# Kernel optimization log

Hardware: AMD Instinct MI355X
Metric: run time of the kernel (lower is better)

The kernel has to match this reference:

```python
import jax, jax.numpy as jnp
import numpy as np
from math import factorial, sqrt

# ---- static configuration (mirrors init_kwargs) ----
IRREPS = [(32, 0), (32, 1), (16, 2)]  # (mul, l); parity of each irrep is (-1)**l (0e,1o,2e)
N_NODES = 200000
DIMS = [m * (2 * l + 1) for m, l in IRREPS]
TOTAL_DIM = sum(DIMS)
OFFS = [0]
for d in DIMS:
    OFFS.append(OFFS[-1] + d)

# ---- real-basis Wigner 3j (same construction as e3nn.o3.wigner_3j) ----
def _cg(j1, m1, j2, m2, j3, m3):
    # su(2) Clebsch-Gordan coefficient <j1 m1 j2 m2 | j3 m3> (Racah formula)
    if m3 != m1 + m2:
        return 0.0
    f = factorial
    pref = sqrt((2 * j3 + 1) * f(j3 + j1 - j2) * f(j3 - j1 + j2) * f(j1 + j2 - j3) / f(j1 + j2 + j3 + 1))
    pref *= sqrt(f(j3 + m3) * f(j3 - m3) * f(j1 - m1) * f(j1 + m1) * f(j2 - m2) * f(j2 + m2))
    s = 0.0
    for k in range(max(0, j2 - j3 - m1, j1 - j3 + m2), min(j1 + j2 - j3, j1 - m1, j2 + m2) + 1):
        s += (-1) ** k / (f(k) * f(j1 + j2 - j3 - k) * f(j1 - m1 - k) * f(j2 + m2 - k) * f(j3 - j2 + m1 + k) * f(j3 - j1 - m2 + k))
    return pref * s

def _q(l):
    # change of basis real <-> complex spherical harmonics, with (-i)**l phase (e3nn convention)
    q = np.zeros((2 * l + 1, 2 * l + 1), dtype=complex)
    for m in range(-l, 0):
        q[l + m, l + abs(m)] = 1 / np.sqrt(2)
        q[l + m, l - abs(m)] = -1j / np.sqrt(2)
    q[l, l] = 1.0
    for m in range(1, l + 1):
        q[l + m, l + abs(m)] = (-1) ** m / np.sqrt(2)
        q[l + m, l - abs(m)] = 1j * (-1) ** m / np.sqrt(2)
    return (-1j) ** l * q

def _w3j(l1, l2, l3):
    C = np.zeros((2 * l1 + 1, 2 * l2 + 1, 2 * l3 + 1))
    for m1 in range(-l1, l1 + 1):
        for m2 in range(-l2, l2 + 1):
            m3 = m1 + m2
            if abs(m3) <= l3:
                C[l1 + m1, l2 + m2, l3 + m3] = _cg(l1, m1, l2, m2, l3, m3)
    W = np.einsum('ai,bj,ck,abc->ijk', _q(l1), _q(l2), np.conj(_q(l3)), C.astype(complex))
    W = np.real(W)
    return (W / np.linalg.norm(W)).astype(np.float32)  # unit Frobenius norm, like e3nn

# ---- enumerate fully-connected TP paths: |l1-l2|<=l3<=l1+l2 and parity match ((-1)**l irreps => l1+l2+l3 even) ----
PATHS = []
for i, (m1, l1) in enumerate(IRREPS):
    for j, (m2, l2) in enumerate(IRREPS):
        for k, (m3, l3) in enumerate(IRREPS):
            if abs(l1 - l2) <= l3 <= l1 + l2 and (l1 + l2 + l3) % 2 == 0:
                PATHS.append((i, j, k))

W3J = {}
for (i, j, k) in PATHS:
    key = (IRREPS[i][1], IRREPS[j][1], IRREPS[k][1])
    if key not in W3J:
        W3J[key] = jnp.asarray(_w3j(*key))

# e3nn normalization: irrep_normalization='component', path_normalization='element', 'uvw' connectivity
FAN = [0] * len(IRREPS)
for (i, j, k) in PATHS:
    FAN[k] += IRREPS[i][0] * IRREPS[j][0]
PATH_COEFF = [sqrt((2 * IRREPS[k][1] + 1) / FAN[k]) for (i, j, k) in PATHS]

TP_WSIZE = sum(IRREPS[i][0] * IRREPS[j][0] * IRREPS[k][0] for (i, j, k) in PATHS)
LIN_WSIZE = sum(m * m for m, l in IRREPS)


def _forward(x, tp_w, lin_w):
    # split x into per-irrep segments [n, mul, 2l+1]
    segs = [x[:, OFFS[i]:OFFS[i + 1]].reshape(-1, IRREPS[i][0], 2 * IRREPS[i][1] + 1)
            for i in range(len(IRREPS))]
    out = [jnp.zeros((x.shape[0], m, 2 * l + 1), x.dtype) for m, l in IRREPS]
    # FullyConnectedTensorProduct(x, x): one CG contraction per path
    off = 0
    for (i, j, k), coeff in zip(PATHS, PATH_COEFF):
        m1, l1 = IRREPS[i]; m2, l2 = IRREPS[j]; m3, l3 = IRREPS[k]
        n = m1 * m2 * m3
        w = tp_w[off:off + n].reshape(m1, m2, m3); off += n
        C = W3J[(l1, l2, l3)]
        out[k] = out[k] + coeff * jnp.einsum('uvw,ijk,zui,zvj->zwk', w, C, segs[i], segs[j])
    # o3.Linear skip: per-irrep channel mixing, 1/sqrt(fan_in) normalization
    loff = 0
    for idx, (m, l) in enumerate(IRREPS):
        w = lin_w[loff:loff + m * m].reshape(m, m); loff += m * m
        out[idx] = out[idx] + jnp.einsum('uw,zui->zwi', w, segs[idx]) / sqrt(m)
    return jnp.concatenate([o.reshape(o.shape[0], -1) for o in out], axis=1)


def setup_inputs() -> dict:
    key = jax.random.key(0)
    k1, k2, k3 = jax.random.split(key, 3)
    return {
        "x": jax.random.normal(k1, (N_NODES, TOTAL_DIM), dtype=jnp.float32),
        "tp_w": jax.random.normal(k2, (TP_WSIZE,), dtype=jnp.float32),
        "lin_w": jax.random.normal(k3, (LIN_WSIZE,), dtype=jnp.float32),
    }


def reference(x, tp_w, lin_w):
    return _forward(x, tp_w, lin_w)
```

## Files before the change

### kernel.cpp

```cpp
#include <hip/hip_runtime.h>

#define T000 0
#define T011 1
#define T101 10
#define T110 19
#define T022 28
#define T202 53
#define T220 78
#define T121 103
#define T211 148
#define T112 193
#define T222 238
#define NTAB 363

#define TP000 0
#define TP011 32768
#define TP022 65536
#define TP101 73728
#define TP110 106496
#define TP112 139264
#define TP121 155648
#define TP202 172032
#define TP211 180224
#define TP220 196608
#define TP222 204800
#define TPEND 208896

#define OFF_CW000 512
#define OFF_CW110 17408
#define OFF_CW220 34304
#define OFF_CW011 38656
#define OFF_CW121 71424
#define OFF_CW022 87808
#define OFF_CW112 96000
#define OFF_CW222 104448
#define OFF_LIN0  106624
#define OFF_LIN1  107648
#define OFF_LIN2  108672
#define PREP_THREADS 108416
#define XT_BYTE_OFF ((size_t)1 << 20)

struct cplx { double re, im; };
__device__ inline cplx cmul(cplx a, cplx b){ return {a.re*b.re - a.im*b.im, a.re*b.im + a.im*b.re}; }

__device__ double dfact(int n){ double r=1; for(int i=2;i<=n;i++) r*=i; return r; }

__device__ double dcgc(int j1,int m1,int j2,int m2,int j3,int m3){
  if (m3 != m1+m2) return 0.0;
  double pref = sqrt((2.0*j3+1)*dfact(j3+j1-j2)*dfact(j3-j1+j2)*dfact(j1+j2-j3)/dfact(j1+j2+j3+1));
  pref *= sqrt(dfact(j3+m3)*dfact(j3-m3)*dfact(j1-m1)*dfact(j1+m1)*dfact(j2-m2)*dfact(j2+m2));
  int k0 = max(0, max(j2-j3-m1, j1-j3+m2));
  int k1 = min(j1+j2-j3, min(j1-m1, j2+m2));
  double s = 0.0;
  for(int k=k0;k<=k1;k++){
    double d = dfact(k)*dfact(j1+j2-j3-k)*dfact(j1-m1-k)*dfact(j2+m2-k)*dfact(j3-j2+m1+k)*dfact(j3-j1-m2+k);
    s += ((k&1)?-1.0:1.0)/d;
  }
  return pref*s;
}

__device__ cplx qel(int l, int a, int c){
  const double s2 = 0.7071067811865475244;
  cplx base = {0.0, 0.0};
  if (a < l){
    if (c == 2*l-a) base = {s2, 0.0};
    else if (c == a) base = {0.0, -s2};
  } else if (a == l){
    if (c == l) base = {1.0, 0.0};
  } else {
    double sgn = ((a-l)&1)? -1.0 : 1.0;
    if (c == a) base = {sgn*s2, 0.0};
    else if (c == 2*l-a) base = {0.0, sgn*s2};
  }
  cplx ph = {1.0,0.0}, mi = {0.0,-1.0};
  for(int t=0;t<l;t++) ph = cmul(ph, mi);
  return cmul(base, ph);
}

__global__ void w3j_init(float* __restrict__ ws){
  __shared__ double red[128];
  __shared__ double snorm;
  const int spec[11][4] = {
    {0,0,0,T000},{0,1,1,T011},{1,0,1,T101},{1,1,0,T110},
    {0,2,2,T022},{2,0,2,T202},{2,2,0,T220},{1,2,1,T121},
    {2,1,1,T211},{1,1,2,T112},{2,2,2,T222}};
  int tbl = blockIdx.x;
  int l1 = spec[tbl][0], l2 = spec[tbl][1], l3 = spec[tbl][2], off = spec[tbl][3];
  int n1 = 2*l1+1, n2 = 2*l2+1, n3 = 2*l3+1, nel = n1*n2*n3;
  int t = threadIdx.x;
  double val = 0.0;
  if (t < nel){
    int k = t % n3, j = (t/n3) % n2, i = t/(n3*n2);
    for(int a=0;a<n1;a++){ int m1 = a-l1;
      for(int b=0;b<n2;b++){ int m2 = b-l2, m3 = m1+m2;
        if (m3 < -l3 || m3 > l3) continue;
        double C = dcgc(l1,m1,l2,m2,l3,m3);
        if (C == 0.0) continue;
        cplx q1 = qel(l1,a,i), q2 = qel(l2,b,j), q3 = qel(l3,l3+m3,k);
        q3.im = -q3.im;
        cplx p = cmul(cmul(q1,q2), q3);
        val += p.re * C;
      }
    }
  }
  red[t] = val*val;
  __syncthreads();
  for(int s=64; s>0; s>>=1){
    if (t < s) red[t] += red[t+s];
    __syncthreads();
  }
  if (t == 0) snorm = sqrt(red[0]);
  __syncthreads();
  if (t < nel) ws[off + t] = (float)(val / snorm);
}

__device__ inline void pdec(int pid, int m, int& u, int& v){
  int uu = 0;
  while (pid >= m-uu){ pid -= (m-uu); uu++; }
  u = uu; v = uu + pid;
}

__global__ void prep3(const float* __restrict__ tp, const float* __restrict__ lin,
                      float* __restrict__ ws){
  const float PK0 = 1.0f/48.0f;
  const float PK1 = 1.0f/32.0f;
  const float PK2 = sqrtf(5.0f)/48.0f;
  int t = blockIdx.x*256 + threadIdx.x;
  if (t >= PREP_THREADS) return;
  if (t < 16896){
    int w = t & 31, pid = t >> 5; int u,v; pdec(pid,32,u,v);
    float s = tp[TP000+(u*32+v)*32+w];
    if (u < v) s += tp[TP000+(v*32+u)*32+w];
    ws[OFF_CW000 + t] = PK0 * ws[T000] * s; return;
  }
  t -= 16896;
  if (t < 16896){
    int w = t & 31, pid = t >> 5; int u,v; pdec(pid,32,u,v);
    float s = tp[TP110+(u*32+v)*32+w];
    if (u < v) s += tp[TP110+(v*32+u)*32+w];
    ws[OFF_CW110 + 16896 + t - 16896] = PK0 * ws[T110] * s;
    return;
  }
  t -= 16896;
  if (t < 4352){
    int w = t & 31, pid = t >> 5; int u,v; pdec(pid,16,u,v);
    float s = tp[TP220+(u*16+v)*32+w];
    if (u < v) s += tp[TP220+(v*16+u)*32+w];
    ws[OFF_CW220 + t] = PK0 * ws[T220] * s; return;
  }
  t -= 4352;
  if (t < 32768){
    int w = t & 31, r = t >> 5; int p = r & 31, q = r >> 5;
    float d011 = ws[T011], d101 = ws[T101];
    float s = d011 * tp[TP011+(p*32+q)*32+w] + d101 * tp[TP101+(q*32+p)*32+w];
    ws[OFF_CW011 + t] = PK1 * s; return;
  }
  t -= 32768;
  if (t < 16384){
    int w = t & 31, r = t >> 5; int q = r & 31, b = r >> 5;
    float s = tp[TP121+(q*16+b)*32+w] + tp[TP211+(b*32+q)*32+w];
    ws[OFF_CW121 + t] = PK1 * s; return;
  }
  t -= 16384;
  if (t < 8192){
    int w = t & 15, r = t >> 4; int p = r & 31, b = r >> 5;
    float d022 = ws[T022], d202 = ws[T202];
    float s = d022 * tp[TP022+(p*16+b)*16+w] + d202 * tp[TP202+(b*32+p)*16+w];
    ws[OFF_CW022 + t] = PK2 * s; return;
  }
  t -= 8192;
  if (t < 8448){
    int w = t & 15, pid = t >> 4; int u,v; pdec(pid,32,u,v);
    float s = tp[TP112+(u*32+v)*16+w];
    if (u < v) s += tp[TP112+(v*32+u)*16+w];
    ws[OFF_CW112 + t] = PK2 * s; return;
  }
  t -= 8448;
  if (t < 2176){
    int w = t & 15, pid = t >> 4; int u,v; pdec(pid,16,u,v);
    float s = tp[TP222+(u*16+v)*16+w];
    if (u < v) s += tp[TP222+(v*16+u)*16+w];
    ws[OFF_CW222 + t] = PK2 * s; return;
  }
  t -= 2176;
  if (t < 1024){ ws[OFF_LIN0 + t] = 0.17677669529663687f * lin[t]; return; }
  t -= 1024;
  if (t < 1024){ ws[OFF_LIN1 + t] = 0.17677669529663687f * lin[1024+t]; return; }
  t -= 1024;
  ws[OFF_LIN2 + t] = 0.25f * lin[2048+t];
}

__global__ void transpose_kernel(const float* __restrict__ x, float* __restrict__ xt, int N){
  __shared__ float tile[64*209];
  int z0 = blockIdx.x*64;
  int nz = N - z0; if (nz > 64) nz = 64;
  for(int idx=threadIdx.x; idx<64*208; idx+=256){
    int zl = idx/208, d = idx - zl*208;
    float v = (zl < nz) ? x[(size_t)z0*208 + idx] : 0.f;
    tile[zl*209 + d] = v;
  }
  __syncthreads();
  for(int idx=threadIdx.x; idx<64*208; idx+=256){
    int d = idx>>6, zl = idx & 63;
    if (zl < nz) xt[(size_t)d*N + z0 + zl] = tile[zl*209 + d];
  }
}

__global__ __launch_bounds__(256, 4)
void tp_fused(const float* __restrict__ xt, const float* __restrict__ ws,
              float* __restrict__ out, int N, int NB){
  __shared__ float sT[NTAB];
  for(int i=threadIdx.x; i<NTAB; i+=256) sT[i] = ws[i];
  __syncthreads();
  int phase = blockIdx.x / NB;
  int z = (blockIdx.x % NB)*256 + threadIdx.x;
  if (z >= N) return;
  const size_t Ns = (size_t)N;
#define XT(d) xt[(size_t)(d)*Ns + z]
  float* __restrict__ oz = out + (size_t)z*208;

  if (phase == 0){
    float acc[32];
#pragma unroll
    for(int w=0;w<32;w++) acc[w]=0.f;
    const float* wp = ws + OFF_CW000;
#pragma unroll 1
    for(int u=0;u<32;u++){
      float su = XT(u);
#pragma unroll 1
      for(int v=u;v<32;v++){
        float p = su * XT(v);
#pragma unroll
        for(int w=0;w<32;w++) acc[w] = fmaf(p, wp[w], acc[w]);
        wp += 32;
      }
    }
    const float* lw = ws + OFF_LIN0;
#pragma unroll 1
    for(int u=0;u<32;u++){
      float su = XT(u);
#pragma unroll
      for(int w=0;w<32;w++) acc[w] = fmaf(su, lw[w], acc[w]);
      lw += 32;
    }
    wp = ws + OFF_CW110;
#pragma unroll 1
    for(int u=0;u<32;u++){
      float a0=XT(32+3*u), a1=XT(33+3*u), a2=XT(34+3*u);
#pragma unroll 1
      for(int v=u;v<32;v++){
        float p = a0*XT(32+3*v) + a1*XT(33+3*v) + a2*XT(34+3*v);
#pragma unroll
        for(int w=0;w<32;w++) acc[w] = fmaf(p, wp[w], acc[w]);
        wp += 32;
      }
    }
    wp = ws + OFF_CW220;
#pragma unroll 1
    for(int u=0;u<16;u++){
      float b0=XT(128+5*u),b1=XT(129+5*u),b2=XT(130+5*u),b3=XT(131+5*u),b4=XT(132+5*u);
#pragma unroll 1
      for(int v=u;v<16;v++){
        float p = b0*XT(128+5*v)+b1*XT(129+5*v)+b2*XT(130+5*v)+b3*XT(131+5*v)+b4*XT(132+5*v);
#pragma unroll
        for(int w=0;w<32;w++) acc[w] = fmaf(p, wp[w], acc[w]);
        wp += 32;
      }
    }
#pragma unroll
    for(int w=0;w<32;w++) oz[w] = acc[w];

  } else if (phase == 1){
    float acc[96];
#pragma unroll
    for(int i=0;i<96;i++) acc[i]=0.f;
    const float* wp = ws + OFF_CW011;
#pragma unroll 1
    for(int q=0;q<32;q++){
      float vq0=XT(32+3*q), vq1=XT(33+3*q), vq2=XT(34+3*q);
#pragma unroll 1
      for(int p=0;p<32;p++){
        float sp = XT(p);
        float p0=sp*vq0, p1=sp*vq1, p2=sp*vq2;
#pragma unroll
        for(int w=0;w<32;w++){
          float wt = wp[w];
          acc[3*w  ] = fmaf(p0, wt, acc[3*w  ]);
          acc[3*w+1] = fmaf(p1, wt, acc[3*w+1]);
          acc[3*w+2] = fmaf(p2, wt, acc[3*w+2]);
        }
        wp += 32;
      }
    }
    wp = ws + OFF_CW121;
#pragma unroll 1
    for(int b=0;b<16;b++){
      float t0=XT(128+5*b),t1=XT(129+5*b),t2=XT(130+5*b),t3=XT(131+5*b),t4=XT(132+5*b);
      float q9[9];
#pragma unroll
      for(int a=0;a<3;a++)
#pragma unroll
        for(int c=0;c<3;c++){
          float s = sT[T121+(a*5+0)*3+c]*t0 + sT[T121+(a*5+1)*3+c]*t1
                  + sT[T121+(a*5+2)*3+c]*t2 + sT[T121+(a*5+3)*3+c]*t3
                  + sT[T121+(a*5+4)*3+c]*t4;
          q9[a*3+c] = s;
        }
#pragma unroll 1
      for(int q=0;q<32;q++){
        float v0=XT(32+3*q), v1=XT(33+3*q), v2=XT(34+3*q);
        float p0 = v0*q9[0] + v1*q9[3] + v2*q9[6];
        float p1 = v0*q9[1] + v1*q9[4] + v2*q9[7];
        float p2 = v0*q9[2] + v1*q9[5] + v2*q9[8];
#pragma unroll
        for(int w=0;w<32;w++){
          float wt = wp[w];
          acc[3*w  ] = fmaf(p0, wt, acc[3*w  ]);
          acc[3*w+1] = fmaf(p1, wt, acc[3*w+1]);
          acc[3*w+2] = fmaf(p2, wt, acc[3*w+2]);
        }
        wp += 32;
      }
    }
    const float* lw = ws + OFF_LIN1;
#pragma unroll 1
    for(int u=0;u<32;u++){
      float v0=XT(32+3*u), v1=XT(33+3*u), v2=XT(34+3*u);
#pragma unroll
      for(int w=0;w<32;w++){
        float wt = lw[w];
        acc[3*w  ] = fmaf(v0, wt, acc[3*w  ]);
        acc[3*w+1] = fmaf(v1, wt, acc[3*w+1]);
        acc[3*w+2] = fmaf(v2, wt, acc[3*w+2]);
      }
      lw += 32;
    }
#pragma unroll
    for(int i=0;i<96;i++) oz[32+i] = acc[i];

  } else {
    float acc[80];
#pragma unroll
    for(int i=0;i<80;i++) acc[i]=0.f;
    const float* wp = ws + OFF_CW022;
#pragma unroll 1
    for(int b=0;b<16;b++){
      float t0=XT(128+5*b),t1=XT(129+5*b),t2=XT(130+5*b),t3=XT(131+5*b),t4=XT(132+5*b);
#pragma unroll 1
      for(int p=0;p<32;p++){
        float sp = XT(p);
        float p0=sp*t0,p1=sp*t1,p2=sp*t2,p3=sp*t3,p4=sp*t4;
#pragma unroll
        for(int w=0;w<16;w++){
          float wt = wp[w];
          acc[5*w  ] = fmaf(p0, wt, acc[5*w  ]);
          acc[5*w+1] = fmaf(p1, wt, acc[5*w+1]);
          acc[5*w+2] = fmaf(p2, wt, acc[5*w+2]);
          acc[5*w+3] = fmaf(p3, wt, acc[5*w+3]);
          acc[5*w+4] = fmaf(p4, wt, acc[5*w+4]);
        }
        wp += 16;
      }
    }
    wp = ws + OFF_CW222;
#pragma unroll 1
    for(int u=0;u<16;u++){
      float tu[5];
#pragma unroll
      for(int j=0;j<5;j++) tu[j]=XT(128+5*u+j);
      float r[25];
#pragma unroll
      for(int b=0;b<5;b++)
#pragma unroll
        for(int c=0;c<5;c++){
          float s=0.f;
#pragma unroll
          for(int a=0;a<5;a++) s = fmaf(sT[T222+(a*5+b)*5+c], tu[a], s);
          r[b*5+c]=s;
        }
#pragma unroll 1
      for(int v=u;v<16;v++){
        float s0=XT(128+5*v),s1=XT(129+5*v),s2=XT(130+5*v),s3=XT(131+5*v),s4=XT(132+5*v);
        float p[5];
#pragma unroll
        for(int c=0;c<5;c++) p[c] = s0*r[c]+s1*r[5+c]+s2*r[10+c]+s3*r[15+c]+s4*r[20+c];
#pragma unroll
        for(int w=0;w<16;w++){
          float wt = wp[w];
#pragma unroll
          for(int c=0;c<5;c++) acc[5*w+c] = fmaf(p[c], wt, acc[5*w+c]);
        }
        wp += 16;
      }
    }
    const float* lw = ws + OFF_LIN2;
#pragma unroll 1
    for(int u=0;u<16;u++){
      float t0=XT(128+5*u),t1=XT(129+5*u),t2=XT(130+5*u),t3=XT(131+5*u),t4=XT(132+5*u);
#pragma unroll
      for(int w=0;w<16;w++){
        float wt = lw[w];
        acc[5*w  ] = fmaf(t0, wt, acc[5*w  ]);
        acc[5*w+1] = fmaf(t1, wt, acc[5*w+1]);
        acc[5*w+2] = fmaf(t2, wt, acc[5*w+2]);
        acc[5*w+3] = fmaf(t3, wt, acc[5*w+3]);
        acc[5*w+4] = fmaf(t4, wt, acc[5*w+4]);
      }
      lw += 16;
    }
    wp = ws + OFF_CW112;
#pragma unroll 1
    for(int u=0;u<32;u++){
      float u0=XT(32+3*u), u1=XT(33+3*u), u2=XT(34+3*u);
      float r[15];
#pragma unroll
      for(int b=0;b<3;b++)
#pragma unroll
        for(int c=0;c<5;c++)
          r[b*5+c] = sT[T112+(0*3+b)*5+c]*u0 + sT[T112+(1*3+b)*5+c]*u1
                   + sT[T112+(2*3+b)*5+c]*u2;
#pragma unroll 1
      for(int v=u;v<32;v++){
        float v0=XT(32+3*v), v1=XT(33+3*v), v2=XT(34+3*v);
        float p[5];
#pragma unroll
        for(int c=0;c<5;c++) p[c] = v0*r[c] + v1*r[5+c] + v2*r[10+c];
#pragma unroll
        for(int w=0;w<16;w++){
          float wt = wp[w];
#pragma unroll
          for(int c=0;c<5;c++) acc[5*w+c] = fmaf(p[c], wt, acc[5*w+c]);
        }
        wp += 16;
      }
    }
#pragma unroll
    for(int i=0;i<80;i++) oz[128+i] = acc[i];
  }
#undef XT
}

extern "C" void kernel_launch(void* const* d_in, const int* in_sizes, int n_in,
                              void* d_out, int out_size, void* d_ws, size_t ws_size,
                              hipStream_t stream) {
  const float* x   = (const float*)d_in[0];
  const float* tpw = (const float*)d_in[1];
  const float* lnw = (const float*)d_in[2];
  float* out = (float*)d_out;
  float* ws  = (float*)d_ws;
  const int N = in_sizes[0]/208;
  const int NB = (N + 255)/256;

  w3j_init<<<11, 128, 0, stream>>>(ws);
  prep3<<<(PREP_THREADS+255)/256, 256, 0, stream>>>(tpw, lnw, ws);

  float* xt = (float*)((char*)d_ws + XT_BYTE_OFF);
  transpose_kernel<<<(N+63)/64, 256, 0, stream>>>(x, xt, N);
  tp_fused<<<3*NB, 256, 0, stream>>>(xt, ws, out, N, NB);
}
```

Before: 2.782 ms.

## Split l=1 and l=2 output phases in half and interleave phase blocks

The l=1 and l=2 output computations are each split by output channel into two halves, so the kernel runs five phases instead of three. Each phase needs fewer accumulators, which lowers register pressure and balances work across blocks. Blocks are interleaved by node (phase = blockIdx % 5), so blocks working on the same nodes share transposed input in cache. Weight tables are re-laid out in prep to match the new blocked loop order (q and b tiles of 4, u pairs for path 112). The cost is that each phase re-reads its inputs and recomputes the CG intermediates.

```diff
diff --git a/kernel.cpp b/kernel.cpp
--- a/kernel.cpp
+++ b/kernel.cpp
@@ -24,7 +24,6 @@
 #define TP211 180224
 #define TP220 196608
 #define TP222 204800
-#define TPEND 208896
 
 #define OFF_CW000 512
 #define OFF_CW110 17408
@@ -138,8 +137,7 @@
     int w = t & 31, pid = t >> 5; int u,v; pdec(pid,32,u,v);
     float s = tp[TP110+(u*32+v)*32+w];
     if (u < v) s += tp[TP110+(v*32+u)*32+w];
-    ws[OFF_CW110 + 16896 + t - 16896] = PK0 * ws[T110] * s;
-    return;
+    ws[OFF_CW110 + t] = PK0 * ws[T110] * s; return;
   }
   t -= 16896;
   if (t < 4352){
@@ -150,34 +148,55 @@
   }
   t -= 4352;
   if (t < 32768){
-    int w = t & 31, r = t >> 5; int p = r & 31, q = r >> 5;
+    int wl = t & 15, ql = (t>>4)&3, p = (t>>6)&31, qt = (t>>11)&7, h = t>>14;
+    int q = 4*qt + ql, w = 16*h + wl;
     float d011 = ws[T011], d101 = ws[T101];
     float s = d011 * tp[TP011+(p*32+q)*32+w] + d101 * tp[TP101+(q*32+p)*32+w];
     ws[OFF_CW011 + t] = PK1 * s; return;
   }
   t -= 32768;
   if (t < 16384){
-    int w = t & 31, r = t >> 5; int q = r & 31, b = r >> 5;
+    int wl = t & 15, ql = (t>>4)&3, b = (t>>6)&15, qt = (t>>10)&7, h = t>>13;
+    int q = 4*qt + ql, w = 16*h + wl;
     float s = tp[TP121+(q*16+b)*32+w] + tp[TP211+(b*32+q)*32+w];
     ws[OFF_CW121 + t] = PK1 * s; return;
   }
   t -= 16384;
   if (t < 8192){
-    int w = t & 15, r = t >> 4; int p = r & 31, b = r >> 5;
+    int wl = t & 7, bl = (t>>3)&3, p = (t>>5)&31, bt = (t>>10)&3, h = t>>12;
+    int b = 4*bt + bl, w = 8*h + wl;
     float d022 = ws[T022], d202 = ws[T202];
     float s = d022 * tp[TP022+(p*16+b)*16+w] + d202 * tp[TP202+(b*32+p)*16+w];
     ws[OFF_CW022 + t] = PK2 * s; return;
   }
   t -= 8192;
   if (t < 8448){
-    int w = t & 15, pid = t >> 4; int u,v; pdec(pid,32,u,v);
+    int h = t / 4224, r = t - 4224*h;
+    int e = r >> 3, wl = r & 7, w = 8*h + wl;
+    int ut = 0;
+    while (ut < 15){
+      int nxt = 65*(ut+1) - 2*(ut+1)*(ut+1);
+      if (e >= nxt) ut++; else break;
+    }
+    int k = e - (65*ut - 2*ut*ut);
+    int u, v;
+    if (k < 3){
+      if (k == 0){ u = 2*ut;         v = 2*ut;   }
+      else       { u = 2*ut + (k-1); v = 2*ut+1; }
+    } else {
+      int k2 = k - 3;
+      v = 2*ut + 2 + (k2 >> 1);
+      u = 2*ut + (k2 & 1);
+    }
     float s = tp[TP112+(u*32+v)*16+w];
     if (u < v) s += tp[TP112+(v*32+u)*16+w];
     ws[OFF_CW112 + t] = PK2 * s; return;
   }
   t -= 8448;
   if (t < 2176){
-    int w = t & 15, pid = t >> 4; int u,v; pdec(pid,16,u,v);
+    int h = t / 1088, r = t - 1088*h;
+    int pid = r >> 3, wl = r & 7, w = 8*h + wl;
+    int u,v; pdec(pid,16,u,v);
     float s = tp[TP222+(u*16+v)*16+w];
     if (u < v) s += tp[TP222+(v*16+u)*16+w];
     ws[OFF_CW222 + t] = PK2 * s; return;
@@ -212,8 +231,8 @@
   __shared__ float sT[NTAB];
   for(int i=threadIdx.x; i<NTAB; i+=256) sT[i] = ws[i];
   __syncthreads();
-  int phase = blockIdx.x / NB;
-  int z = (blockIdx.x % NB)*256 + threadIdx.x;
+  int phase = blockIdx.x % 5;
+  int z = (blockIdx.x / 5)*256 + threadIdx.x;
   if (z >= N) return;
   const size_t Ns = (size_t)N;
 #define XT(d) xt[(size_t)(d)*Ns + z]
@@ -270,64 +289,69 @@
 #pragma unroll
     for(int w=0;w<32;w++) oz[w] = acc[w];
 
-  } else if (phase == 1){
-    float acc[96];
-#pragma unroll
-    for(int i=0;i<96;i++) acc[i]=0.f;
-    const float* wp = ws + OFF_CW011;
-#pragma unroll 1
-    for(int q=0;q<32;q++){
-      float vq0=XT(32+3*q), vq1=XT(33+3*q), vq2=XT(34+3*q);
-#pragma unroll 1
-      for(int p=0;p<32;p++){
+  } else if (phase <= 2){
+    const int h = phase - 1;
+    float acc[48];
+#pragma unroll
+    for(int i=0;i<48;i++) acc[i]=0.f;
+    const float* wp011 = ws + OFF_CW011 + (h<<14);
+    const float* wp121 = ws + OFF_CW121 + (h<<13);
+#pragma unroll 1
+    for(int qt=0; qt<8; ++qt){
+      float vq[12];
+#pragma unroll
+      for(int j=0;j<12;j++) vq[j] = XT(32 + 12*qt + j);
+#pragma unroll 1
+      for(int p=0; p<32; ++p){
         float sp = XT(p);
-        float p0=sp*vq0, p1=sp*vq1, p2=sp*vq2;
-#pragma unroll
-        for(int w=0;w<32;w++){
-          float wt = wp[w];
-          acc[3*w  ] = fmaf(p0, wt, acc[3*w  ]);
-          acc[3*w+1] = fmaf(p1, wt, acc[3*w+1]);
-          acc[3*w+2] = fmaf(p2, wt, acc[3*w+2]);
+#pragma unroll
+        for(int ql=0; ql<4; ++ql){
+          float p0 = sp*vq[3*ql], p1 = sp*vq[3*ql+1], p2 = sp*vq[3*ql+2];
+#pragma unroll
+          for(int w=0; w<16; ++w){
+            float wt = wp011[ql*16+w];
+            acc[3*w  ] = fmaf(p0, wt, acc[3*w  ]);
+            acc[3*w+1] = fmaf(p1, wt, acc[3*w+1]);
+            acc[3*w+2] = fmaf(p2, wt, acc[3*w+2]);
+          }
         }
-        wp += 32;
-      }
-    }
-    wp = ws + OFF_CW121;
-#pragma unroll 1
-    for(int b=0;b<16;b++){
-      float t0=XT(128+5*b),t1=XT(129+5*b),t2=XT(130+5*b),t3=XT(131+5*b),t4=XT(132+5*b);
-      float q9[9];
-#pragma unroll
-      for(int a=0;a<3;a++)
-#pragma unroll
-        for(int c=0;c<3;c++){
-          float s = sT[T121+(a*5+0)*3+c]*t0 + sT[T121+(a*5+1)*3+c]*t1
-                  + sT[T121+(a*5+2)*3+c]*t2 + sT[T121+(a*5+3)*3+c]*t3
-                  + sT[T121+(a*5+4)*3+c]*t4;
-          q9[a*3+c] = s;
+        wp011 += 64;
+      }
+#pragma unroll 1
+      for(int b=0; b<16; ++b){
+        float t0=XT(128+5*b), t1=XT(129+5*b), t2=XT(130+5*b), t3=XT(131+5*b), t4=XT(132+5*b);
+        float q9[9];
+#pragma unroll
+        for(int a=0;a<3;a++)
+#pragma unroll
+          for(int c=0;c<3;c++){
+            q9[a*3+c] = sT[T121+(a*5+0)*3+c]*t0 + sT[T121+(a*5+1)*3+c]*t1
+                      + sT[T121+(a*5+2)*3+c]*t2 + sT[T121+(a*5+3)*3+c]*t3
+                      + sT[T121+(a*5+4)*3+c]*t4;
+          }
+#pragma unroll
+        for(int ql=0; ql<4; ++ql){
+          float v0=vq[3*ql], v1=vq[3*ql+1], v2=vq[3*ql+2];
+          float p0 = v0*q9[0] + v1*q9[3] + v2*q9[6];
+          float p1 = v0*q9[1] + v1*q9[4] + v2*q9[7];
+          float p2 = v0*q9[2] + v1*q9[5] + v2*q9[8];
+#pragma unroll
+          for(int w=0; w<16; ++w){
+            float wt = wp121[ql*16+w];
+            acc[3*w  ] = fmaf(p0, wt, acc[3*w  ]);
+            acc[3*w+1] = fmaf(p1, wt, acc[3*w+1]);
+            acc[3*w+2] = fmaf(p2, wt, acc[3*w+2]);
+          }
         }
-#pragma unroll 1
-      for(int q=0;q<32;q++){
-        float v0=XT(32+3*q), v1=XT(33+3*q), v2=XT(34+3*q);
-        float p0 = v0*q9[0] + v1*q9[3] + v2*q9[6];
-        float p1 = v0*q9[1] + v1*q9[4] + v2*q9[7];
-        float p2 = v0*q9[2] + v1*q9[5] + v2*q9[8];
-#pragma unroll
-        for(int w=0;w<32;w++){
-          float wt = wp[w];
-          acc[3*w  ] = fmaf(p0, wt, acc[3*w  ]);
-          acc[3*w+1] = fmaf(p1, wt, acc[3*w+1]);
-          acc[3*w+2] = fmaf(p2, wt, acc[3*w+2]);
-        }
-        wp += 32;
-      }
-    }
-    const float* lw = ws + OFF_LIN1;
-#pragma unroll 1
-    for(int u=0;u<32;u++){
+        wp121 += 64;
+      }
+    }
+    const float* lw = ws + OFF_LIN1 + 16*h;
+#pragma unroll 1
+    for(int u=0; u<32; ++u){
       float v0=XT(32+3*u), v1=XT(33+3*u), v2=XT(34+3*u);
 #pragma unroll
-      for(int w=0;w<32;w++){
+      for(int w=0; w<16; ++w){
         float wt = lw[w];
         acc[3*w  ] = fmaf(v0, wt, acc[3*w  ]);
         acc[3*w+1] = fmaf(v1, wt, acc[3*w+1]);
@@ -336,35 +360,41 @@
       lw += 32;
     }
 #pragma unroll
-    for(int i=0;i<96;i++) oz[32+i] = acc[i];
+    for(int i=0;i<48;i++) oz[32 + 48*h + i] = acc[i];
 
   } else {
-    float acc[80];
-#pragma unroll
-    for(int i=0;i<80;i++) acc[i]=0.f;
-    const float* wp = ws + OFF_CW022;
-#pragma unroll 1
-    for(int b=0;b<16;b++){
-      float t0=XT(128+5*b),t1=XT(129+5*b),t2=XT(130+5*b),t3=XT(131+5*b),t4=XT(132+5*b);
-#pragma unroll 1
-      for(int p=0;p<32;p++){
+    const int h = phase - 3;
+    float acc[40];
+#pragma unroll
+    for(int i=0;i<40;i++) acc[i]=0.f;
+    const float* wp = ws + OFF_CW022 + (h<<12);
+#pragma unroll 1
+    for(int bt=0; bt<4; ++bt){
+      float tt[20];
+#pragma unroll
+      for(int j=0;j<20;j++) tt[j] = XT(128 + 20*bt + j);
+#pragma unroll 1
+      for(int p=0; p<32; ++p){
         float sp = XT(p);
-        float p0=sp*t0,p1=sp*t1,p2=sp*t2,p3=sp*t3,p4=sp*t4;
-#pragma unroll
-        for(int w=0;w<16;w++){
-          float wt = wp[w];
-          acc[5*w  ] = fmaf(p0, wt, acc[5*w  ]);
-          acc[5*w+1] = fmaf(p1, wt, acc[5*w+1]);
-          acc[5*w+2] = fmaf(p2, wt, acc[5*w+2]);
-          acc[5*w+3] = fmaf(p3, wt, acc[5*w+3]);
-          acc[5*w+4] = fmaf(p4, wt, acc[5*w+4]);
+#pragma unroll
+        for(int bl=0; bl<4; ++bl){
+          float p0=sp*tt[5*bl], p1=sp*tt[5*bl+1], p2=sp*tt[5*bl+2], p3=sp*tt[5*bl+3], p4=sp*tt[5*bl+4];
+#pragma unroll
+          for(int w=0; w<8; ++w){
+            float wt = wp[bl*8+w];
+            acc[5*w  ] = fmaf(p0, wt, acc[5*w  ]);
+            acc[5*w+1] = fmaf(p1, wt, acc[5*w+1]);
+            acc[5*w+2] = fmaf(p2, wt, acc[5*w+2]);
+            acc[5*w+3] = fmaf(p3, wt, acc[5*w+3]);
+            acc[5*w+4] = fmaf(p4, wt, acc[5*w+4]);
+          }
         }
-        wp += 16;
-      }
-    }
-    wp = ws + OFF_CW222;
-#pragma unroll 1
-    for(int u=0;u<16;u++){
+        wp += 32;
+      }
+    }
+    wp = ws + OFF_CW222 + h*1088;
+#pragma unroll 1
+    for(int u=0; u<16; ++u){
       float tu[5];
 #pragma unroll
       for(int j=0;j<5;j++) tu[j]=XT(128+5*u+j);
@@ -379,26 +409,26 @@
           r[b*5+c]=s;
         }
 #pragma unroll 1
-      for(int v=u;v<16;v++){
+      for(int v=u; v<16; ++v){
         float s0=XT(128+5*v),s1=XT(129+5*v),s2=XT(130+5*v),s3=XT(131+5*v),s4=XT(132+5*v);
         float p[5];
 #pragma unroll
         for(int c=0;c<5;c++) p[c] = s0*r[c]+s1*r[5+c]+s2*r[10+c]+s3*r[15+c]+s4*r[20+c];
 #pragma unroll
-        for(int w=0;w<16;w++){
+        for(int w=0; w<8; ++w){
           float wt = wp[w];
 #pragma unroll
           for(int c=0;c<5;c++) acc[5*w+c] = fmaf(p[c], wt, acc[5*w+c]);
         }
-        wp += 16;
-      }
-    }
-    const float* lw = ws + OFF_LIN2;
-#pragma unroll 1
-    for(int u=0;u<16;u++){
+        wp += 8;
+      }
+    }
+    const float* lw = ws + OFF_LIN2 + 8*h;
+#pragma unroll 1
+    for(int u=0; u<16; ++u){
       float t0=XT(128+5*u),t1=XT(129+5*u),t2=XT(130+5*u),t3=XT(131+5*u),t4=XT(132+5*u);
 #pragma unroll
-      for(int w=0;w<16;w++){
+      for(int w=0; w<8; ++w){
         float wt = lw[w];
         acc[5*w  ] = fmaf(t0, wt, acc[5*w  ]);
         acc[5*w+1] = fmaf(t1, wt, acc[5*w+1]);
@@ -408,34 +438,64 @@
       }
       lw += 16;
     }
-    wp = ws + OFF_CW112;
-#pragma unroll 1
-    for(int u=0;u<32;u++){
-      float u0=XT(32+3*u), u1=XT(33+3*u), u2=XT(34+3*u);
-      float r[15];
-#pragma unroll
-      for(int b=0;b<3;b++)
-#pragma unroll
-        for(int c=0;c<5;c++)
-          r[b*5+c] = sT[T112+(0*3+b)*5+c]*u0 + sT[T112+(1*3+b)*5+c]*u1
-                   + sT[T112+(2*3+b)*5+c]*u2;
-#pragma unroll 1
-      for(int v=u;v<32;v++){
+    wp = ws + OFF_CW112 + h*4224;
+#pragma unroll 1
+    for(int ut=0; ut<16; ++ut){
+      float uu[6];
+#pragma unroll
+      for(int j=0;j<6;j++) uu[j] = XT(32 + 6*ut + j);
+      float r2[30];
+#pragma unroll
+      for(int ul=0; ul<2; ++ul)
+#pragma unroll
+        for(int b=0;b<3;b++)
+#pragma unroll
+          for(int c=0;c<5;c++)
+            r2[ul*15+b*5+c] = sT[T112+(0*3+b)*5+c]*uu[3*ul]
+                            + sT[T112+(1*3+b)*5+c]*uu[3*ul+1]
+                            + sT[T112+(2*3+b)*5+c]*uu[3*ul+2];
+      {
+        float p[5];
+#pragma unroll
+        for(int c=0;c<5;c++) p[c] = uu[0]*r2[c] + uu[1]*r2[5+c] + uu[2]*r2[10+c];
+#pragma unroll
+        for(int w=0;w<8;w++){ float wt = wp[w];
+#pragma unroll
+          for(int c=0;c<5;c++) acc[5*w+c] = fmaf(p[c], wt, acc[5*w+c]); }
+        wp += 8;
+#pragma unroll
+        for(int c=0;c<5;c++) p[c] = uu[3]*r2[c] + uu[4]*r2[5+c] + uu[5]*r2[10+c];
+#pragma unroll
+        for(int w=0;w<8;w++){ float wt = wp[w];
+#pragma unroll
+          for(int c=0;c<5;c++) acc[5*w+c] = fmaf(p[c], wt, acc[5*w+c]); }
+        wp += 8;
+#pragma unroll
+        for(int c=0;c<5;c++) p[c] = uu[3]*r2[15+c] + uu[4]*r2[20+c] + uu[5]*r2[25+c];
+#pragma unroll
+        for(int w=0;w<8;w++){ float wt = wp[w];
+#pragma unroll
+          for(int c=0;c<5;c++) acc[5*w+c] = fmaf(p[c], wt, acc[5*w+c]); }
+        wp += 8;
+      }
+#pragma unroll 1
+      for(int v=2*ut+2; v<32; ++v){
         float v0=XT(32+3*v), v1=XT(33+3*v), v2=XT(34+3*v);
-        float p[5];
-#pragma unroll
-        for(int c=0;c<5;c++) p[c] = v0*r[c] + v1*r[5+c] + v2*r[10+c];
-#pragma unroll
-        for(int w=0;w<16;w++){
-          float wt = wp[w];
-#pragma unroll
-          for(int c=0;c<5;c++) acc[5*w+c] = fmaf(p[c], wt, acc[5*w+c]);
+#pragma unroll
+        for(int ul=0; ul<2; ++ul){
+          float p[5];
+#pragma unroll
+          for(int c=0;c<5;c++) p[c] = v0*r2[ul*15+c] + v1*r2[ul*15+5+c] + v2*r2[ul*15+10+c];
+#pragma unroll
+          for(int w=0;w<8;w++){ float wt = wp[w];
+#pragma unroll
+            for(int c=0;c<5;c++) acc[5*w+c] = fmaf(p[c], wt, acc[5*w+c]); }
+          wp += 8;
         }
-        wp += 16;
-      }
-    }
-#pragma unroll
-    for(int i=0;i<80;i++) oz[128+i] = acc[i];
+      }
+    }
+#pragma unroll
+    for(int i=0;i<40;i++) oz[128 + 40*h + i] = acc[i];
   }
 #undef XT
 }
@@ -456,5 +516,5 @@
 
   float* xt = (float*)((char*)d_ws + XT_BYTE_OFF);
   transpose_kernel<<<(N+63)/64, 256, 0, stream>>>(x, xt, N);
-  tp_fused<<<3*NB, 256, 0, stream>>>(xt, ws, out, N, NB);
-}
+  tp_fused<<<5*NB, 256, 0, stream>>>(xt, ws, out, N, NB);
+}
```

Result: slower. 3.035 ms (+9.1%).

## Fuse transpose into TP kernel with LDS-staged nodes and wave-split output channels

Applied to the files above, without the earlier changes.

Removes the separate transpose pass and global transposed buffer. Each block now loads 64 nodes into LDS in a padded column layout, and each of the four waves computes one slice of the output channels for all three output irreps. Per-thread accumulators shrink from up to 96 to 8–24 registers, weights are read as float4, and outputs are stored as float4. The trade-off is that every wave reads the shared x values once per slice, and the 54KB of LDS per block limits occupancy.

```diff
diff --git a/kernel.cpp b/kernel.cpp
--- a/kernel.cpp
+++ b/kernel.cpp
@@ -24,7 +24,6 @@
 #define TP211 180224
 #define TP220 196608
 #define TP222 204800
-#define TPEND 208896
 
 #define OFF_CW000 512
 #define OFF_CW110 17408
@@ -38,7 +37,6 @@
 #define OFF_LIN1  107648
 #define OFF_LIN2  108672
 #define PREP_THREADS 108416
-#define XT_BYTE_OFF ((size_t)1 << 20)
 
 struct cplx { double re, im; };
 __device__ inline cplx cmul(cplx a, cplx b){ return {a.re*b.re - a.im*b.im, a.re*b.im + a.im*b.re}; }
@@ -138,8 +136,7 @@
     int w = t & 31, pid = t >> 5; int u,v; pdec(pid,32,u,v);
     float s = tp[TP110+(u*32+v)*32+w];
     if (u < v) s += tp[TP110+(v*32+u)*32+w];
-    ws[OFF_CW110 + 16896 + t - 16896] = PK0 * ws[T110] * s;
-    return;
+    ws[OFF_CW110 + t] = PK0 * ws[T110] * s; return;
   }
   t -= 16896;
   if (t < 4352){
@@ -190,255 +187,244 @@
   ws[OFF_LIN2 + t] = 0.25f * lin[2048+t];
 }
 
-__global__ void transpose_kernel(const float* __restrict__ x, float* __restrict__ xt, int N){
-  __shared__ float tile[64*209];
-  int z0 = blockIdx.x*64;
+#define XL(d) xL[(d)*65 + lane]
+
+__global__ __launch_bounds__(256, 3)
+void tp_block(const float* __restrict__ x, const float* __restrict__ ws,
+              float* __restrict__ out, int N){
+  __shared__ float xL[208*65];
+  const int z0 = blockIdx.x * 64;
+  const int tid = threadIdx.x;
   int nz = N - z0; if (nz > 64) nz = 64;
-  for(int idx=threadIdx.x; idx<64*208; idx+=256){
-    int zl = idx/208, d = idx - zl*208;
-    float v = (zl < nz) ? x[(size_t)z0*208 + idx] : 0.f;
-    tile[zl*209 + d] = v;
+  for (int i = tid; i < 64*208; i += 256){
+    int zl = i / 208, d = i - zl*208;
+    float v = (zl < nz) ? x[(size_t)z0*208 + i] : 0.f;
+    xL[d*65 + zl] = v;
   }
   __syncthreads();
-  for(int idx=threadIdx.x; idx<64*208; idx+=256){
-    int d = idx>>6, zl = idx & 63;
-    if (zl < nz) xt[(size_t)d*N + z0 + zl] = tile[zl*209 + d];
-  }
-}
-
-__global__ __launch_bounds__(256, 4)
-void tp_fused(const float* __restrict__ xt, const float* __restrict__ ws,
-              float* __restrict__ out, int N, int NB){
-  __shared__ float sT[NTAB];
-  for(int i=threadIdx.x; i<NTAB; i+=256) sT[i] = ws[i];
-  __syncthreads();
-  int phase = blockIdx.x / NB;
-  int z = (blockIdx.x % NB)*256 + threadIdx.x;
-  if (z >= N) return;
-  const size_t Ns = (size_t)N;
-#define XT(d) xt[(size_t)(d)*Ns + z]
-  float* __restrict__ oz = out + (size_t)z*208;
-
-  if (phase == 0){
-    float acc[32];
-#pragma unroll
-    for(int w=0;w<32;w++) acc[w]=0.f;
-    const float* wp = ws + OFF_CW000;
+  const int wsl  = tid >> 6;
+  const int lane = tid & 63;
+  if (lane >= nz) return;
+  float* __restrict__ oz = out + (size_t)(z0 + lane)*208;
+
+  {
+    float acc[8];
+#pragma unroll
+    for(int i=0;i<8;i++) acc[i]=0.f;
+#define FMA8(P) { \
+    acc[0]=fmaf(P,wA.x,acc[0]); acc[1]=fmaf(P,wA.y,acc[1]); \
+    acc[2]=fmaf(P,wA.z,acc[2]); acc[3]=fmaf(P,wA.w,acc[3]); \
+    acc[4]=fmaf(P,wB.x,acc[4]); acc[5]=fmaf(P,wB.y,acc[5]); \
+    acc[6]=fmaf(P,wB.z,acc[6]); acc[7]=fmaf(P,wB.w,acc[7]); }
+    const float* wp = ws + OFF_CW000 + wsl*8;
 #pragma unroll 1
     for(int u=0;u<32;u++){
-      float su = XT(u);
-#pragma unroll 1
+      float su = XL(u);
+#pragma unroll 2
       for(int v=u;v<32;v++){
-        float p = su * XT(v);
-#pragma unroll
-        for(int w=0;w<32;w++) acc[w] = fmaf(p, wp[w], acc[w]);
+        float p = su * XL(v);
+        float4 wA = *(const float4*)wp; float4 wB = *(const float4*)(wp+4);
+        FMA8(p)
         wp += 32;
       }
     }
-    const float* lw = ws + OFF_LIN0;
+    const float* lw = ws + OFF_LIN0 + wsl*8;
 #pragma unroll 1
     for(int u=0;u<32;u++){
-      float su = XT(u);
-#pragma unroll
-      for(int w=0;w<32;w++) acc[w] = fmaf(su, lw[w], acc[w]);
+      float su = XL(u);
+      float4 wA = *(const float4*)lw; float4 wB = *(const float4*)(lw+4);
+      FMA8(su)
       lw += 32;
     }
-    wp = ws + OFF_CW110;
+    wp = ws + OFF_CW110 + wsl*8;
 #pragma unroll 1
     for(int u=0;u<32;u++){
-      float a0=XT(32+3*u), a1=XT(33+3*u), a2=XT(34+3*u);
-#pragma unroll 1
+      float a0=XL(32+3*u), a1=XL(33+3*u), a2=XL(34+3*u);
+#pragma unroll 2
       for(int v=u;v<32;v++){
-        float p = a0*XT(32+3*v) + a1*XT(33+3*v) + a2*XT(34+3*v);
-#pragma unroll
-        for(int w=0;w<32;w++) acc[w] = fmaf(p, wp[w], acc[w]);
+        float p = a0*XL(32+3*v) + a1*XL(33+3*v) + a2*XL(34+3*v);
+        float4 wA = *(const float4*)wp; float4 wB = *(const float4*)(wp+4);
+        FMA8(p)
         wp += 32;
       }
     }
-    wp = ws + OFF_CW220;
+    wp = ws + OFF_CW220 + wsl*8;
 #pragma unroll 1
     for(int u=0;u<16;u++){
-      float b0=XT(128+5*u),b1=XT(129+5*u),b2=XT(130+5*u),b3=XT(131+5*u),b4=XT(132+5*u);
-#pragma unroll 1
+      float b0=XL(128+5*u),b1=XL(129+5*u),b2=XL(130+5*u),b3=XL(131+5*u),b4=XL(132+5*u);
+#pragma unroll 2
       for(int v=u;v<16;v++){
-        float p = b0*XT(128+5*v)+b1*XT(129+5*v)+b2*XT(130+5*v)+b3*XT(131+5*v)+b4*XT(132+5*v);
-#pragma unroll
-        for(int w=0;w<32;w++) acc[w] = fmaf(p, wp[w], acc[w]);
+        float p = b0*XL(128+5*v)+b1*XL(129+5*v)+b2*XL(130+5*v)+b3*XL(131+5*v)+b4*XL(132+5*v);
+        float4 wA = *(const float4*)wp; float4 wB = *(const float4*)(wp+4);
+        FMA8(p)
         wp += 32;
       }
     }
-#pragma unroll
-    for(int w=0;w<32;w++) oz[w] = acc[w];
-
-  } else if (phase == 1){
-    float acc[96];
-#pragma unroll
-    for(int i=0;i<96;i++) acc[i]=0.f;
-    const float* wp = ws + OFF_CW011;
+#undef FMA8
+    float4 s0; s0.x=acc[0]; s0.y=acc[1]; s0.z=acc[2]; s0.w=acc[3];
+    float4 s1; s1.x=acc[4]; s1.y=acc[5]; s1.z=acc[6]; s1.w=acc[7];
+    *(float4*)(oz + wsl*8)     = s0;
+    *(float4*)(oz + wsl*8 + 4) = s1;
+  }
+
+  {
+    float acc[24];
+#pragma unroll
+    for(int i=0;i<24;i++) acc[i]=0.f;
+#define FMA3(J,WT) { float wt_=(WT); \
+    acc[3*(J)  ]=fmaf(p0,wt_,acc[3*(J)  ]); \
+    acc[3*(J)+1]=fmaf(p1,wt_,acc[3*(J)+1]); \
+    acc[3*(J)+2]=fmaf(p2,wt_,acc[3*(J)+2]); }
+#define FMA24 { FMA3(0,wA.x) FMA3(1,wA.y) FMA3(2,wA.z) FMA3(3,wA.w) \
+                FMA3(4,wB.x) FMA3(5,wB.y) FMA3(6,wB.z) FMA3(7,wB.w) }
+    const float* wp = ws + OFF_CW011 + wsl*8;
 #pragma unroll 1
     for(int q=0;q<32;q++){
-      float vq0=XT(32+3*q), vq1=XT(33+3*q), vq2=XT(34+3*q);
-#pragma unroll 1
+      float vq0=XL(32+3*q), vq1=XL(33+3*q), vq2=XL(34+3*q);
+#pragma unroll 2
       for(int p=0;p<32;p++){
-        float sp = XT(p);
+        float sp = XL(p);
         float p0=sp*vq0, p1=sp*vq1, p2=sp*vq2;
-#pragma unroll
-        for(int w=0;w<32;w++){
-          float wt = wp[w];
-          acc[3*w  ] = fmaf(p0, wt, acc[3*w  ]);
-          acc[3*w+1] = fmaf(p1, wt, acc[3*w+1]);
-          acc[3*w+2] = fmaf(p2, wt, acc[3*w+2]);
+        float4 wA = *(const float4*)wp; float4 wB = *(const float4*)(wp+4);
+        FMA24
+        wp += 32;
+      }
+    }
+    wp = ws + OFF_CW121 + wsl*8;
+#pragma unroll 1
+    for(int b=0;b<16;b++){
+      float t0=XL(128+5*b), t1=XL(129+5*b), t2=XL(130+5*b), t3=XL(131+5*b), t4=XL(132+5*b);
+      float q9[9];
+#pragma unroll
+      for(int a=0;a<3;a++)
+#pragma unroll
+        for(int c=0;c<3;c++){
+          q9[a*3+c] = ws[T121+(a*5+0)*3+c]*t0 + ws[T121+(a*5+1)*3+c]*t1
+                    + ws[T121+(a*5+2)*3+c]*t2 + ws[T121+(a*5+3)*3+c]*t3
+                    + ws[T121+(a*5+4)*3+c]*t4;
         }
-        wp += 32;
-      }
-    }
-    wp = ws + OFF_CW121;
-#pragma unroll 1
-    for(int b=0;b<16;b++){
-      float t0=XT(128+5*b),t1=XT(129+5*b),t2=XT(130+5*b),t3=XT(131+5*b),t4=XT(132+5*b);
-      float q9[9];
-#pragma unroll
-      for(int a=0;a<3;a++)
-#pragma unroll
-        for(int c=0;c<3;c++){
-          float s = sT[T121+(a*5+0)*3+c]*t0 + sT[T121+(a*5+1)*3+c]*t1
-                  + sT[T121+(a*5+2)*3+c]*t2 + sT[T121+(a*5+3)*3+c]*t3
-                  + sT[T121+(a*5+4)*3+c]*t4;
-          q9[a*3+c] = s;
-        }
-#pragma unroll 1
+#pragma unroll 2
       for(int q=0;q<32;q++){
-        float v0=XT(32+3*q), v1=XT(33+3*q), v2=XT(34+3*q);
+        float v0=XL(32+3*q), v1=XL(33+3*q), v2=XL(34+3*q);
         float p0 = v0*q9[0] + v1*q9[3] + v2*q9[6];
         float p1 = v0*q9[1] + v1*q9[4] + v2*q9[7];
         float p2 = v0*q9[2] + v1*q9[5] + v2*q9[8];
-#pragma unroll
-        for(int w=0;w<32;w++){
-          float wt = wp[w];
-          acc[3*w  ] = fmaf(p0, wt, acc[3*w  ]);
-          acc[3*w+1] = fmaf(p1, wt, acc[3*w+1]);
-          acc[3*w+2] = fmaf(p2, wt, acc[3*w+2]);
+        float4 wA = *(const float4*)wp; float4 wB = *(const float4*)(wp+4);
+        FMA24
+        wp += 32;
+      }
+    }
+    const float* lw = ws + OFF_LIN1 + wsl*8;
+#pragma unroll 1
+    for(int u=0;u<32;u++){
+      float p0=XL(32+3*u), p1=XL(33+3*u), p2=XL(34+3*u);
+      float4 wA = *(const float4*)lw; float4 wB = *(const float4*)(lw+4);
+      FMA24
+      lw += 32;
+    }
+#undef FMA24
+#undef FMA3
+    float* ob = oz + 32 + wsl*24;
+#pragma unroll
+    for(int j=0;j<6;j++){
+      float4 s; s.x=acc[4*j]; s.y=acc[4*j+1]; s.z=acc[4*j+2]; s.w=acc[4*j+3];
+      *(float4*)(ob + 4*j) = s;
+    }
+  }
+
+  {
+    float acc[20];
+#pragma unroll
+    for(int i=0;i<20;i++) acc[i]=0.f;
+#define FMA5(J,WT) { float wt_=(WT); \
+    acc[5*(J)  ]=fmaf(p0,wt_,acc[5*(J)  ]); \
+    acc[5*(J)+1]=fmaf(p1,wt_,acc[5*(J)+1]); \
+    acc[5*(J)+2]=fmaf(p2,wt_,acc[5*(J)+2]); \
+    acc[5*(J)+3]=fmaf(p3,wt_,acc[5*(J)+3]); \
+    acc[5*(J)+4]=fmaf(p4,wt_,acc[5*(J)+4]); }
+#define FMA20 { FMA5(0,wA.x) FMA5(1,wA.y) FMA5(2,wA.z) FMA5(3,wA.w) }
+    const float* wp = ws + OFF_CW022 + wsl*4;
+#pragma unroll 1
+    for(int b=0;b<16;b++){
+      float t0=XL(128+5*b), t1=XL(129+5*b), t2=XL(130+5*b), t3=XL(131+5*b), t4=XL(132+5*b);
+#pragma unroll 2
+      for(int p=0;p<32;p++){
+        float sp = XL(p);
+        float p0=sp*t0, p1=sp*t1, p2=sp*t2, p3=sp*t3, p4=sp*t4;
+        float4 wA = *(const float4*)wp;
+        FMA20
+        wp += 16;
+      }
+    }
+    wp = ws + OFF_CW222 + wsl*4;
+#pragma unroll 1
+    for(int u=0;u<16;u++){
+      float tu0=XL(128+5*u), tu1=XL(129+5*u), tu2=XL(130+5*u), tu3=XL(131+5*u), tu4=XL(132+5*u);
+      float r[25];
+#pragma unroll
+      for(int b=0;b<5;b++)
+#pragma unroll
+        for(int c=0;c<5;c++){
+          r[b*5+c] = ws[T222+(0*5+b)*5+c]*tu0 + ws[T222+(1*5+b)*5+c]*tu1
+                   + ws[T222+(2*5+b)*5+c]*tu2 + ws[T222+(3*5+b)*5+c]*tu3
+                   + ws[T222+(4*5+b)*5+c]*tu4;
         }
-        wp += 32;
-      }
-    }
-    const float* lw = ws + OFF_LIN1;
+#pragma unroll 2
+      for(int v=u;v<16;v++){
+        float s0=XL(128+5*v),s1=XL(129+5*v),s2=XL(130+5*v),s3=XL(131+5*v),s4=XL(132+5*v);
+        float p0 = s0*r[0]+s1*r[5]+s2*r[10]+s3*r[15]+s4*r[20];
+        float p1 = s0*r[1]+s1*r[6]+s2*r[11]+s3*r[16]+s4*r[21];
+        float p2 = s0*r[2]+s1*r[7]+s2*r[12]+s3*r[17]+s4*r[22];
+        float p3 = s0*r[3]+s1*r[8]+s2*r[13]+s3*r[18]+s4*r[23];
+        float p4 = s0*r[4]+s1*r[9]+s2*r[14]+s3*r[19]+s4*r[24];
+        float4 wA = *(const float4*)wp;
+        FMA20
+        wp += 16;
+      }
+    }
+    const float* lw = ws + OFF_LIN2 + wsl*4;
+#pragma unroll 1
+    for(int u=0;u<16;u++){
+      float p0=XL(128+5*u), p1=XL(129+5*u), p2=XL(130+5*u), p3=XL(131+5*u), p4=XL(132+5*u);
+      float4 wA = *(const float4*)lw;
+      FMA20
+      lw += 16;
+    }
+    wp = ws + OFF_CW112 + wsl*4;
 #pragma unroll 1
     for(int u=0;u<32;u++){
-      float v0=XT(32+3*u), v1=XT(33+3*u), v2=XT(34+3*u);
-#pragma unroll
-      for(int w=0;w<32;w++){
-        float wt = lw[w];
-        acc[3*w  ] = fmaf(v0, wt, acc[3*w  ]);
-        acc[3*w+1] = fmaf(v1, wt, acc[3*w+1]);
-        acc[3*w+2] = fmaf(v2, wt, acc[3*w+2]);
-      }
-      lw += 32;
-    }
-#pragma unroll
-    for(int i=0;i<96;i++) oz[32+i] = acc[i];
-
-  } else {
-    float acc[80];
-#pragma unroll
-    for(int i=0;i<80;i++) acc[i]=0.f;
-    const float* wp = ws + OFF_CW022;
-#pragma unroll 1
-    for(int b=0;b<16;b++){
-      float t0=XT(128+5*b),t1=XT(129+5*b),t2=XT(130+5*b),t3=XT(131+5*b),t4=XT(132+5*b);
-#pragma unroll 1
-      for(int p=0;p<32;p++){
-        float sp = XT(p);
-        float p0=sp*t0,p1=sp*t1,p2=sp*t2,p3=sp*t3,p4=sp*t4;
-#pragma unroll
-        for(int w=0;w<16;w++){
-          float wt = wp[w];
-          acc[5*w  ] = fmaf(p0, wt, acc[5*w  ]);
-          acc[5*w+1] = fmaf(p1, wt, acc[5*w+1]);
-          acc[5*w+2] = fmaf(p2, wt, acc[5*w+2]);
-          acc[5*w+3] = fmaf(p3, wt, acc[5*w+3]);
-          acc[5*w+4] = fmaf(p4, wt, acc[5*w+4]);
-        }
+      float u0=XL(32+3*u), u1=XL(33+3*u), u2=XL(34+3*u);
+      float r[15];
+#pragma unroll
+      for(int b=0;b<3;b++)
+#pragma unroll
+        for(int c=0;c<5;c++)
+          r[b*5+c] = ws[T112+(0*3+b)*5+c]*u0 + ws[T112+(1*3+b)*5+c]*u1
+                   + ws[T112+(2*3+b)*5+c]*u2;
+#pragma unroll 2
+      for(int v=u;v<32;v++){
+        float v0=XL(32+3*v), v1=XL(33+3*v), v2=XL(34+3*v);
+        float p0 = v0*r[0]+v1*r[5]+v2*r[10];
+        float p1 = v0*r[1]+v1*r[6]+v2*r[11];
+        float p2 = v0*r[2]+v1*r[7]+v2*r[12];
+        float p3 = v0*r[3]+v1*r[8]+v2*r[13];
+        float p4 = v0*r[4]+v1*r[9]+v2*r[14];
+        float4 wA = *(const float4*)wp;
+        FMA20
         wp += 16;
       }
     }
-    wp = ws + OFF_CW222;
-#pragma unroll 1
-    for(int u=0;u<16;u++){
-      float tu[5];
-#pragma unroll
-      for(int j=0;j<5;j++) tu[j]=XT(128+5*u+j);
-      float r[25];
-#pragma unroll
-      for(int b=0;b<5;b++)
-#pragma unroll
-        for(int c=0;c<5;c++){
-          float s=0.f;
-#pragma unroll
-          for(int a=0;a<5;a++) s = fmaf(sT[T222+(a*5+b)*5+c], tu[a], s);
-          r[b*5+c]=s;
-        }
-#pragma unroll 1
-      for(int v=u;v<16;v++){
-        float s0=XT(128+5*v),s1=XT(129+5*v),s2=XT(130+5*v),s3=XT(131+5*v),s4=XT(132+5*v);
-        float p[5];
-#pragma unroll
-        for(int c=0;c<5;c++) p[c] = s0*r[c]+s1*r[5+c]+s2*r[10+c]+s3*r[15+c]+s4*r[20+c];
-#pragma unroll
-        for(int w=0;w<16;w++){
-          float wt = wp[w];
-#pragma unroll
-          for(int c=0;c<5;c++) acc[5*w+c] = fmaf(p[c], wt, acc[5*w+c]);
-        }
-        wp += 16;
-      }
-    }
-    const float* lw = ws + OFF_LIN2;
-#pragma unroll 1
-    for(int u=0;u<16;u++){
-      float t0=XT(128+5*u),t1=XT(129+5*u),t2=XT(130+5*u),t3=XT(131+5*u),t4=XT(132+5*u);
-#pragma unroll
-      for(int w=0;w<16;w++){
-        float wt = lw[w];
-        acc[5*w  ] = fmaf(t0, wt, acc[5*w  ]);
-        acc[5*w+1] = fmaf(t1, wt, acc[5*w+1]);
-        acc[5*w+2] = fmaf(t2, wt, acc[5*w+2]);
-        acc[5*w+3] = fmaf(t3, wt, acc[5*w+3]);
-        acc[5*w+4] = fmaf(t4, wt, acc[5*w+4]);
-      }
-      lw += 16;
-    }
-    wp = ws + OFF_CW112;
-#pragma unroll 1
-    for(int u=0;u<32;u++){
-      float u0=XT(32+3*u), u1=XT(33+3*u), u2=XT(34+3*u);
-      float r[15];
-#pragma unroll
-      for(int b=0;b<3;b++)
-#pragma unroll
-        for(int c=0;c<5;c++)
-          r[b*5+c] = sT[T112+(0*3+b)*5+c]*u0 + sT[T112+(1*3+b)*5+c]*u1
-                   + sT[T112+(2*3+b)*5+c]*u2;
-#pragma unroll 1
-      for(int v=u;v<32;v++){
-        float v0=XT(32+3*v), v1=XT(33+3*v), v2=XT(34+3*v);
-        float p[5];
-#pragma unroll
-        for(int c=0;c<5;c++) p[c] = v0*r[c] + v1*r[5+c] + v2*r[10+c];
-#pragma unroll
-        for(int w=0;w<16;w++){
-          float wt = wp[w];
-#pragma unroll
-          for(int c=0;c<5;c++) acc[5*w+c] = fmaf(p[c], wt, acc[5*w+c]);
-        }
-        wp += 16;
-      }
-    }
-#pragma unroll
-    for(int i=0;i<80;i++) oz[128+i] = acc[i];
-  }
-#undef XT
-}
+#undef FMA20
+#undef FMA5
+    float* ob = oz + 128 + wsl*20;
+#pragma unroll
+    for(int j=0;j<5;j++){
+      float4 s; s.x=acc[4*j]; s.y=acc[4*j+1]; s.z=acc[4*j+2]; s.w=acc[4*j+3];
+      *(float4*)(ob + 4*j) = s;
+    }
+  }
+}
+#undef XL
 
 extern "C" void kernel_launch(void* const* d_in, const int* in_sizes, int n_in,
                               void* d_out, int out_size, void* d_ws, size_t ws_size,
@@ -449,12 +435,8 @@
   float* out = (float*)d_out;
   float* ws  = (float*)d_ws;
   const int N = in_sizes[0]/208;
-  const int NB = (N + 255)/256;
 
   w3j_init<<<11, 128, 0, stream>>>(ws);
   prep3<<<(PREP_THREADS+255)/256, 256, 0, stream>>>(tpw, lnw, ws);
-
-  float* xt = (float*)((char*)d_ws + XT_BYTE_OFF);
-  transpose_kernel<<<(N+63)/64, 256, 0, stream>>>(x, xt, N);
-  tp_fused<<<3*NB, 256, 0, stream>>>(xt, ws, out, N, NB);
-}
+  tp_block<<<(N+63)/64, 256, 0, stream>>>(x, ws, out, N);
+}
```

New measurement: 4.288 ms. 1.54x slower.
